# Optimization experiments

Measured on AMD Instinct MI355X. Metric: run time of the kernel, lower is better.

## Reference

```python
import jax, jax.numpy as jnp
import numpy as np

N_NODES = 100000
N_EDGES = 1600000
D = 128


def setup_inputs() -> dict:
    key = jax.random.key(0)
    ks = jax.random.split(key, 8)
    s = lambda fan_in: 1.0 / np.sqrt(fan_in)
    return {
        "node_feature": jax.random.normal(ks[0], (N_NODES, D), dtype=jnp.float32),
        "src": jax.random.randint(ks[1], (N_EDGES,), 0, N_NODES),
        "dst": jax.random.randint(ks[2], (N_EDGES,), 0, N_NODES),
        "W1": jax.random.normal(ks[3], (2 * D, D), dtype=jnp.float32) * s(2 * D),
        "b1": jnp.zeros((D,), dtype=jnp.float32),
        "W2": jax.random.normal(ks[4], (D, D), dtype=jnp.float32) * s(D),
        "b2": jnp.zeros((D,), dtype=jnp.float32),
        "W3": jax.random.normal(ks[5], (D, D), dtype=jnp.float32) * s(D),
        "b3": jnp.zeros((D,), dtype=jnp.float32),
    }


def reference(node_feature, src, dst, W1, b1, W2, b2, W3, b3):
    n_nodes = node_feature.shape[0]
    # message: gather src node features over edges  [E, D]
    msg = node_feature[src]
    # reduce: sum messages into destination nodes   [N, D]
    agg = jax.ops.segment_sum(msg, dst, num_segments=n_nodes)
    # apply: concat(aggregated, own) -> MLP         [N, 2D] -> [N, D]
    inp = jnp.concatenate([agg, node_feature], axis=-1)
    h = jax.nn.relu(inp @ W1 + b1)
    h = jax.nn.relu(h @ W2 + b2)
    return h @ W3 + b3
```

## Files before the change

kernel.cpp:

```cpp
#include <hip/hip_runtime.h>

#define NNODES 100000
#define NEDGES 1600000
#define DD 128
#define BM 32
#define NBUCK 98
#define NBLK_MLP (NNODES / BM)
#define CAP 32
#define CAPB 20480
#define BIN1_WGS 200
#define BIN1_EPW 8192

#define WS_GCUR 100000
#define WS_BBASE 100128
#define WS_OFFS 100352
#define WS_ESRC 201216

#define WT1HI 0
#define WT1LO 32768
#define WT2HI 65536
#define WT2LO 81920
#define WT3HI 98304
#define WT3LO 114688

typedef __attribute__((ext_vector_type(8))) short short8;
typedef __attribute__((ext_vector_type(4))) float f32x4;

__device__ __forceinline__ void bf16_split(float x, ushort& hi, ushort& lo) {
  unsigned u = __float_as_uint(x);
  ushort h = (ushort)((u + 0x7FFFu + ((u >> 16) & 1u)) >> 16);
  float r = x - __uint_as_float(((unsigned)h) << 16);
  unsigned v = __float_as_uint(r);
  ushort l = (ushort)((v + 0x7FFFu + ((v >> 16) & 1u)) >> 16);
  hi = h;
  lo = l;
}

__device__ __forceinline__ void split8(const float4 v0, const float4 v1,
                                       short8& hi, short8& lo) {
  float x[8] = {v0.x, v0.y, v0.z, v0.w, v1.x, v1.y, v1.z, v1.w};
#pragma unroll
  for (int j = 0; j < 8; ++j) {
    ushort h, l;
    bf16_split(x[j], h, l);
    hi[j] = (short)h;
    lo[j] = (short)l;
  }
}

__global__ __launch_bounds__(256) void bin1_kernel(const int* __restrict__ src,
                                                   const int* __restrict__ dst,
                                                   int* __restrict__ gcur,
                                                   unsigned* __restrict__ ebuf) {
  __shared__ unsigned stage[NBUCK][CAP];
  __shared__ int scnt[NBUCK];
  const int t = threadIdx.x;
  for (int i = t; i < NBUCK; i += 256) scnt[i] = 0;
  __syncthreads();
  const int e0 = blockIdx.x * BIN1_EPW;
  for (int r = 0; r < BIN1_EPW / 1024; ++r) {
    unsigned item[4];
    int buck[4];
    int pend[4];
#pragma unroll
    for (int j = 0; j < 4; ++j) {
      pend[j] = 0;
      int e = e0 + r * 1024 + j * 256 + t;
      if (e < NEDGES) {
        int d = dst[e];
        int s = src[e];
        buck[j] = d >> 10;
        item[j] = ((unsigned)(d & 1023) << 17) | (unsigned)s;
        int p = atomicAdd(&scnt[buck[j]], 1);
        if (p < CAP)
          stage[buck[j]][p] = item[j];
        else
          pend[j] = 1;
      }
    }
    int pendLeft;
    do {
      __syncthreads();
      if (t < NBUCK && scnt[t] >= CAP) {
        int base = t * CAPB + atomicAdd(&gcur[t], CAP);
        for (int q = 0; q < CAP; ++q) ebuf[base + q] = stage[t][q];
        scnt[t] = 0;
      }
      __syncthreads();
      int mypend = 0;
#pragma unroll
      for (int j = 0; j < 4; ++j) {
        if (pend[j]) {
          int p = atomicAdd(&scnt[buck[j]], 1);
          if (p < CAP) {
            stage[buck[j]][p] = item[j];
            pend[j] = 0;
          } else {
            mypend = 1;
          }
        }
      }
      pendLeft = __syncthreads_count(mypend);
    } while (pendLeft > 0);
  }
  __syncthreads();
  if (t < NBUCK) {
    int n = scnt[t];
    if (n > 0) {
      int base = t * CAPB + atomicAdd(&gcur[t], n);
      for (int q = 0; q < n; ++q) ebuf[base + q] = stage[t][q];
    }
  }
}

__global__ __launch_bounds__(128) void bscan_kernel(const int* __restrict__ gcur,
                                                    int* __restrict__ bbase,
                                                    int* __restrict__ offs) {
  __shared__ int s[128];
  const int t = threadIdx.x;
  int v = (t < NBUCK) ? gcur[t] : 0;
  s[t] = v;
  __syncthreads();
  for (int off = 1; off < 128; off <<= 1) {
    int u = (t >= off) ? s[t - off] : 0;
    __syncthreads();
    s[t] += u;
    __syncthreads();
  }
  if (t < NBUCK) bbase[t] = s[t] - v;
  if (t == NBUCK - 1) offs[NNODES] = s[t];
}

__global__ __launch_bounds__(1024) void bucket_csr_kernel(const unsigned* __restrict__ ebuf,
                                                          const int* __restrict__ gcur,
                                                          const int* __restrict__ bbase,
                                                          int* __restrict__ offs,
                                                          int* __restrict__ esrc) {
  __shared__ int h[1024];
  __shared__ int cur[1024];
  const int t = threadIdx.x;
  const int c = blockIdx.x;
  const int n = gcur[c];
  const unsigned* eb = ebuf + c * CAPB;
  h[t] = 0;
  __syncthreads();
  for (int i = t; i < n; i += 1024) atomicAdd(&h[eb[i] >> 17], 1);
  __syncthreads();
  int v = h[t];
  for (int off = 1; off < 1024; off <<= 1) {
    int u = (t >= off) ? h[t - off] : 0;
    __syncthreads();
    h[t] += u;
    __syncthreads();
  }
  int excl = h[t] - v + bbase[c];
  int node = (c << 10) + t;
  if (node < NNODES) offs[node] = excl;
  cur[t] = excl;
  __syncthreads();
  for (int i = t; i < n; i += 1024) {
    unsigned e = eb[i];
    int p = atomicAdd(&cur[e >> 17], 1);
    esrc[p] = (int)(e & 0x1FFFFu);
  }
}

__global__ __launch_bounds__(256) void wprep_kernel(const float* __restrict__ W1,
                                                    const float* __restrict__ W2,
                                                    const float* __restrict__ W3,
                                                    ushort* __restrict__ wt) {
  int tid = blockIdx.x * 256 + threadIdx.x;
  const float* W;
  int dstHi, dstLo, k, col;
  if (tid < 32768) {
    int j = tid & 7, l = (tid >> 3) & 63, tile = tid >> 9;
    int kk = tile & 7, c16 = tile >> 3;
    k = kk * 32 + (l >> 4) * 8 + j;
    col = c16 * 16 + (l & 15);
    W = W1;
    dstHi = WT1HI + tid;
    dstLo = WT1LO + tid;
  } else {
    int t2 = tid - 32768;
    int which = t2 >> 14;
    int t1 = t2 & 16383;
    int j = t1 & 7, l = (t1 >> 3) & 63, tile = t1 >> 9;
    int kk = tile & 3, c16 = tile >> 2;
    k = kk * 32 + (l >> 4) * 8 + j;
    col = c16 * 16 + (l & 15);
    W = which ? W3 : W2;
    dstHi = (which ? WT3HI : WT2HI) + t1;
    dstLo = (which ? WT3LO : WT2LO) + t1;
  }
  ushort hi, lo;
  bf16_split(W[k * DD + col], hi, lo);
  wt[dstHi] = hi;
  wt[dstLo] = lo;
}


template <int KT>
__device__ __forceinline__ void lds_ksteps(const ushort* Hh, const ushort* Hl,
                                           const ushort* __restrict__ WhiT,
                                           const ushort* __restrict__ WloT,
                                           int tileOff, int rb, int wc, int lane,
                                           int l15, int lhi, f32x4 acc[4]) {
#pragma unroll 2
  for (int kk = 0; kk < 4; ++kk) {
    int row = rb + l15;
    int byte = (row * 256 + kk * 64 + lhi * 16) ^ ((row & 7) << 4);
    short8 ahi = *(const short8*)((const char*)Hh + byte);
    short8 alo = *(const short8*)((const char*)Hl + byte);
#pragma unroll
    for (int ct = 0; ct < 4; ++ct) {
      int tb = ((wc * 4 + ct) * KT + tileOff + kk) * 512 + lane * 8;
      short8 bhi = *(const short8*)&WhiT[tb];
      short8 blo = *(const short8*)&WloT[tb];
      acc[ct] = __builtin_amdgcn_mfma_f32_16x16x32_bf16(ahi, bhi, acc[ct], 0, 0, 0);
      acc[ct] = __builtin_amdgcn_mfma_f32_16x16x32_bf16(ahi, blo, acc[ct], 0, 0, 0);
      acc[ct] = __builtin_amdgcn_mfma_f32_16x16x32_bf16(alo, bhi, acc[ct], 0, 0, 0);
    }
  }
}

__device__ __forceinline__ void l1_step(const float* __restrict__ srcb,
                                        const ushort* __restrict__ wt,
                                        int kkTile, int kOff, int rowA,
                                        int wc, int lane, int lhi,
                                        f32x4 acc[4]) {
  const float* p = srcb + rowA * DD + kOff + lhi * 8;
  float4 v0 = *(const float4*)p;
  float4 v1 = *(const float4*)(p + 4);
  short8 ahi, alo;
  split8(v0, v1, ahi, alo);
#pragma unroll
  for (int ct = 0; ct < 4; ++ct) {
    int tb = ((wc * 4 + ct) * 8 + kkTile) * 512 + lane * 8;
    short8 bhi = *(const short8*)&wt[WT1HI + tb];
    short8 blo = *(const short8*)&wt[WT1LO + tb];
    acc[ct] = __builtin_amdgcn_mfma_f32_16x16x32_bf16(ahi, bhi, acc[ct], 0, 0, 0);
    acc[ct] = __builtin_amdgcn_mfma_f32_16x16x32_bf16(ahi, blo, acc[ct], 0, 0, 0);
    acc[ct] = __builtin_amdgcn_mfma_f32_16x16x32_bf16(alo, bhi, acc[ct], 0, 0, 0);
  }
}

__device__ __forceinline__ void store_h(ushort* Hh, ushort* Hl,
                                        const float* __restrict__ b,
                                        int rb, int wc, int l15, int lhi,
                                        f32x4 acc[4]) {
#pragma unroll
  for (int ct = 0; ct < 4; ++ct) {
    int col = wc * 64 + ct * 16 + l15;
    float bias = b[col];
#pragma unroll
    for (int i = 0; i < 4; ++i) {
      int row = rb + lhi * 4 + i;
      float v = fmaxf(acc[ct][i] + bias, 0.f);
      ushort h, l;
      bf16_split(v, h, l);
      int byte = (row * 256 + col * 2) ^ ((row & 7) << 4);
      *(ushort*)((char*)Hh + byte) = h;
      *(ushort*)((char*)Hl + byte) = l;
    }
  }
}

__global__ __launch_bounds__(256, 6) void fused_kernel(const float* __restrict__ nf,
                                                       const int* __restrict__ offs,
                                                       const int* __restrict__ esrc,
                                                       const ushort* __restrict__ wt,
                                                       const float* __restrict__ b1,
                                                       const float* __restrict__ b2,
                                                       const float* __restrict__ b3,
                                                       float* __restrict__ out) {
  __shared__ ushort smem[8192];
  ushort* Xhi = smem;
  ushort* Xlo = smem + 4096;

  const int t = threadIdx.x;
  const int lane = t & 63;
  const int w = t >> 6;
  const int rb = (w & 1) * 16;
  const int wc = w >> 1;
  const int l15 = lane & 15;
  const int lhi = lane >> 4;
  const int base = blockIdx.x * BM;

  {
    const int g = t >> 5;
    const int l32 = t & 31;
    const int col = l32 << 2;
    for (int j = 0; j < 4; ++j) {
      const int r = g * 4 + j;
      const int node = base + r;
      float4 a0 = make_float4(0.f, 0.f, 0.f, 0.f);
      float4 a1 = make_float4(0.f, 0.f, 0.f, 0.f);
      float4 a2 = make_float4(0.f, 0.f, 0.f, 0.f);
      float4 a3 = make_float4(0.f, 0.f, 0.f, 0.f);
      const int beg = offs[node];
      const int end = offs[node + 1];
      int i = beg;
      for (; i + 3 < end; i += 4) {
        int s0 = esrc[i];
        int s1 = esrc[i + 1];
        int s2 = esrc[i + 2];
        int s3 = esrc[i + 3];
        float4 v0 = *(const float4*)&nf[s0 * DD + col];
        float4 v1 = *(const float4*)&nf[s1 * DD + col];
        float4 v2 = *(const float4*)&nf[s2 * DD + col];
        float4 v3 = *(const float4*)&nf[s3 * DD + col];
        a0.x += v0.x; a0.y += v0.y; a0.z += v0.z; a0.w += v0.w;
        a1.x += v1.x; a1.y += v1.y; a1.z += v1.z; a1.w += v1.w;
        a2.x += v2.x; a2.y += v2.y; a2.z += v2.z; a2.w += v2.w;
        a3.x += v3.x; a3.y += v3.y; a3.z += v3.z; a3.w += v3.w;
      }
      for (; i < end; ++i) {
        int s0 = esrc[i];
        float4 v0 = *(const float4*)&nf[s0 * DD + col];
        a0.x += v0.x; a0.y += v0.y; a0.z += v0.z; a0.w += v0.w;
      }
      a0.x += a1.x; a0.y += a1.y; a0.z += a1.z; a0.w += a1.w;
      a2.x += a3.x; a2.y += a3.y; a2.z += a3.z; a2.w += a3.w;
      a0.x += a2.x; a0.y += a2.y; a0.z += a2.z; a0.w += a2.w;
      ushort h0, h1, h2, h3, l0, l1, l2, l3;
      bf16_split(a0.x, h0, l0);
      bf16_split(a0.y, h1, l1);
      bf16_split(a0.z, h2, l2);
      bf16_split(a0.w, h3, l3);
      int byte = (r * 256 + col * 2) ^ ((r & 7) << 4);
      *(ushort4*)((char*)Xhi + byte) = make_ushort4(h0, h1, h2, h3);
      *(ushort4*)((char*)Xlo + byte) = make_ushort4(l0, l1, l2, l3);
    }
  }
  __syncthreads();

  const int rowG = base + rb + l15;
  const f32x4 z = {0.f, 0.f, 0.f, 0.f};
  f32x4 acc[4];

#pragma unroll
  for (int ct = 0; ct < 4; ++ct) acc[ct] = z;
  lds_ksteps<8>(Xhi, Xlo, wt + WT1HI, wt + WT1LO, 0, rb, wc, lane, l15, lhi, acc);
#pragma unroll 2
  for (int kk = 0; kk < 4; ++kk)
    l1_step(nf, wt, kk + 4, kk * 32, rowG, wc, lane, lhi, acc);
  __syncthreads();
  store_h(Xhi, Xlo, b1, rb, wc, l15, lhi, acc);
  __syncthreads();

#pragma unroll
  for (int ct = 0; ct < 4; ++ct) acc[ct] = z;
  lds_ksteps<4>(Xhi, Xlo, wt + WT2HI, wt + WT2LO, 0, rb, wc, lane, l15, lhi, acc);
  __syncthreads();
  store_h(Xhi, Xlo, b2, rb, wc, l15, lhi, acc);
  __syncthreads();

#pragma unroll
  for (int ct = 0; ct < 4; ++ct) acc[ct] = z;
  lds_ksteps<4>(Xhi, Xlo, wt + WT3HI, wt + WT3LO, 0, rb, wc, lane, l15, lhi, acc);
#pragma unroll
  for (int ct = 0; ct < 4; ++ct) {
    int col = wc * 64 + ct * 16 + l15;
    float bias = b3[col];
#pragma unroll
    for (int i = 0; i < 4; ++i) {
      int row = base + rb + lhi * 4 + i;
      out[row * DD + col] = acc[ct][i] + bias;
    }
  }
}

extern "C" void kernel_launch(void* const* d_in, const int* in_sizes, int n_in,
                              void* d_out, int out_size, void* d_ws, size_t ws_size,
                              hipStream_t stream) {
  const float* nf = (const float*)d_in[0];
  const int* src = (const int*)d_in[1];
  const int* dst = (const int*)d_in[2];
  const float* W1 = (const float*)d_in[3];
  const float* b1 = (const float*)d_in[4];
  const float* W2 = (const float*)d_in[5];
  const float* b2 = (const float*)d_in[6];
  const float* W3 = (const float*)d_in[7];
  const float* b3 = (const float*)d_in[8];
  float* out = (float*)d_out;

  int* wsi = (int*)d_ws;
  int* gcur = wsi + WS_GCUR;
  int* bbase = wsi + WS_BBASE;
  int* offs = wsi + WS_OFFS;
  int* esrc = wsi + WS_ESRC;
  ushort* wt = (ushort*)wsi;

  unsigned* ebuf = (unsigned*)out;

  hipMemsetAsync(gcur, 0, NBUCK * sizeof(int), stream);
  bin1_kernel<<<BIN1_WGS, 256, 0, stream>>>(src, dst, gcur, ebuf);
  bscan_kernel<<<1, 128, 0, stream>>>(gcur, bbase, offs);
  bucket_csr_kernel<<<NBUCK, 1024, 0, stream>>>(ebuf, gcur, bbase, offs, esrc);
  wprep_kernel<<<256, 256, 0, stream>>>(W1, W2, W3, wt);
  fused_kernel<<<NBLK_MLP, 256, 0, stream>>>(nf, offs, esrc, wt, b1, b2, b3, out);
}
```

Measured before the change: 254.5 us.

## Dynamically assign gather rows to half-waves and software-prefetch edge indices

Replaces the fixed assignment of four rows per 32-thread group with a shared-memory atomic counter, so half-waves pull rows dynamically and balance uneven node degrees. The edge-index loads for the next group of four edges are issued before the current feature loads, shortening the dependent esrc-to-nf latency chain. Launch bounds raise the occupancy target from 6 to 8 blocks per CU, which may force register spilling in the MLP part. The atomic and shuffle add a small per-row cost.

```diff
diff --git a/kernel.cpp b/kernel.cpp
--- a/kernel.cpp
+++ b/kernel.cpp
@@ -265,7 +265,7 @@
   }
 }
 
-__global__ __launch_bounds__(256, 6) void fused_kernel(const float* __restrict__ nf,
+__global__ __launch_bounds__(256, 8) void fused_kernel(const float* __restrict__ nf,
                                                        const int* __restrict__ offs,
                                                        const int* __restrict__ esrc,
                                                        const ushort* __restrict__ wt,
@@ -274,6 +274,7 @@
                                                        const float* __restrict__ b3,
                                                        float* __restrict__ out) {
   __shared__ ushort smem[8192];
+  __shared__ int nextRow;
   ushort* Xhi = smem;
   ushort* Xlo = smem + 4096;
 
@@ -286,12 +287,17 @@
   const int lhi = lane >> 4;
   const int base = blockIdx.x * BM;
 
+  if (t == 0) nextRow = 0;
+  __syncthreads();
+
   {
-    const int g = t >> 5;
     const int l32 = t & 31;
     const int col = l32 << 2;
-    for (int j = 0; j < 4; ++j) {
-      const int r = g * 4 + j;
+    for (;;) {
+      int r;
+      if (l32 == 0) r = atomicAdd(&nextRow, 1);
+      r = __shfl(r, 0, 32);
+      if (r >= BM) break;
       const int node = base + r;
       float4 a0 = make_float4(0.f, 0.f, 0.f, 0.f);
       float4 a1 = make_float4(0.f, 0.f, 0.f, 0.f);
@@ -300,11 +306,13 @@
       const int beg = offs[node];
       const int end = offs[node + 1];
       int i = beg;
-      for (; i + 3 < end; i += 4) {
-        int s0 = esrc[i];
-        int s1 = esrc[i + 1];
-        int s2 = esrc[i + 2];
-        int s3 = esrc[i + 3];
+      int s0, s1, s2, s3;
+      const bool have4 = (i + 3 < end);
+      if (have4) {
+        s0 = esrc[i]; s1 = esrc[i + 1]; s2 = esrc[i + 2]; s3 = esrc[i + 3];
+      }
+      for (; i + 7 < end; i += 4) {
+        int n0 = esrc[i + 4], n1 = esrc[i + 5], n2 = esrc[i + 6], n3 = esrc[i + 7];
         float4 v0 = *(const float4*)&nf[s0 * DD + col];
         float4 v1 = *(const float4*)&nf[s1 * DD + col];
         float4 v2 = *(const float4*)&nf[s2 * DD + col];
@@ -313,10 +321,22 @@
         a1.x += v1.x; a1.y += v1.y; a1.z += v1.z; a1.w += v1.w;
         a2.x += v2.x; a2.y += v2.y; a2.z += v2.z; a2.w += v2.w;
         a3.x += v3.x; a3.y += v3.y; a3.z += v3.z; a3.w += v3.w;
+        s0 = n0; s1 = n1; s2 = n2; s3 = n3;
+      }
+      if (have4) {
+        float4 v0 = *(const float4*)&nf[s0 * DD + col];
+        float4 v1 = *(const float4*)&nf[s1 * DD + col];
+        float4 v2 = *(const float4*)&nf[s2 * DD + col];
+        float4 v3 = *(const float4*)&nf[s3 * DD + col];
+        a0.x += v0.x; a0.y += v0.y; a0.z += v0.z; a0.w += v0.w;
+        a1.x += v1.x; a1.y += v1.y; a1.z += v1.z; a1.w += v1.w;
+        a2.x += v2.x; a2.y += v2.y; a2.z += v2.z; a2.w += v2.w;
+        a3.x += v3.x; a3.y += v3.y; a3.z += v3.z; a3.w += v3.w;
+        i += 4;
       }
       for (; i < end; ++i) {
-        int s0 = esrc[i];
-        float4 v0 = *(const float4*)&nf[s0 * DD + col];
+        int s = esrc[i];
+        float4 v0 = *(const float4*)&nf[s * DD + col];
         a0.x += v0.x; a0.y += v0.y; a0.z += v0.z; a0.w += v0.w;
       }
       a0.x += a1.x; a0.y += a1.y; a0.z += a1.z; a0.w += a1.w;
```

New measurement: 250.6 us. Within noise of the previous version (-1.5%).
